# Kernel optimization log

Hardware: AMD Instinct MI355X
Metric: run time of the kernel (lower is better)

Reference implementation:

```python
import jax, jax.numpy as jnp
import numpy as np
from jax import lax

DX, DY, T, B, NMC, HID = 128, 64, 50, 128, 100, 64
PROC_SD, EMIT_SD, LOC_R = 0.05, 0.1, 5.0


def gaspari_cohn(radius, d):
    # static construction (numpy), matches construct_Gaspari_Cohn
    def G(z):
        if 0 <= z < 1:
            return 1.0 - 5.0/3*z**2 + 5.0/8*z**3 + 0.5*z**4 - 0.25*z**5
        elif 1 <= z < 2:
            return 4.0 - 5.0*z + 5.0/3*z**2 + 5.0/8*z**3 - 0.5*z**4 + 1.0/12*z**5 - 2.0/(3.0*z)
        return 0.0
    t = np.zeros((d, d), dtype=np.float32)
    for i in range(d):
        for j in range(d):
            dist = min(abs(i - j), d - abs(i - j))
            t[i, j] = G(dist / radius)
    return jnp.asarray(t)


def setup_inputs():
    key = jax.random.key(0)
    ks = jax.random.split(key, 16)
    rn = lambda k, s, sc=0.05: (jax.random.normal(k, s) * sc).astype(jnp.float32)
    return {
        'observations': jax.random.normal(ks[0], (B, T, DY), jnp.float32),
        'W1': rn(ks[1], (128, DX)), 'b1': jnp.zeros((128,), jnp.float32),
        'W2': rn(ks[2], (64, 128)), 'b2': jnp.zeros((64,), jnp.float32),
        'W3': rn(ks[3], (32, 64)), 'b3': jnp.zeros((32,), jnp.float32),
        'W4': rn(ks[4], (DX, 32)), 'b4': jnp.zeros((DX,), jnp.float32),
        'Wih': rn(ks[5], (4 * HID, DY)), 'Whh': rn(ks[6], (4 * HID, HID)), 'bih': jnp.zeros((4 * HID,), jnp.float32),
        'Wm': rn(ks[7], (DX, HID)), 'bm': jnp.zeros((DX,), jnp.float32),
        'Wv': rn(ks[8], (DX, HID)), 'bv': jnp.zeros((DX,), jnp.float32),
        'eps0': jax.random.normal(ks[9], (NMC, B, DX), jnp.float32),
        'eps_seq': jax.random.normal(ks[10], (T, NMC, B, DX), jnp.float32),
        'noise_y': jax.random.normal(ks[11], (T, B, DY), jnp.float32),
    }


def _forward(observations, W1, b1, W2, b2, W3, b3, W4, b4,
             Wih, Whh, bih, Wm, bm, Wv, bv, eps0, eps_seq, noise_y):
    dt = observations.dtype
    taper = gaspari_cohn(LOC_R, DX).astype(dt)        # [dx, dx]
    Hm = jnp.eye(DX, dtype=dt)[:DY]                    # [dy, dx] emission matrix
    R = (EMIT_SD ** 2) * jnp.eye(DY, dtype=dt)         # observation noise cov

    def mlp(x):  # Four_Layer_NN, relu, no residual
        h = jax.nn.relu(x @ W1.T + b1)
        h = jax.nn.relu(h @ W2.T + b2)
        h = jax.nn.relu(h @ W3.T + b3)
        return h @ W4.T + b4

    # ---- LSTM recognition net -> q(x0) (diagonal MVN) ----
    def lstm_step(carry, x_t):
        h, c = carry
        g = x_t @ Wih.T + h @ Whh.T + bih
        i, f, gg, o = jnp.split(g, 4, axis=-1)
        c = jax.nn.sigmoid(f) * c + jax.nn.sigmoid(i) * jnp.tanh(gg)
        h = jax.nn.sigmoid(o) * jnp.tanh(c)
        return (h, c), None
    h0 = jnp.zeros((B, HID), dt)
    (h_last, _), _ = lax.scan(lstm_step, (h0, h0), jnp.moveaxis(observations, 1, 0))
    q_mean = h_last @ Wm.T + bm                          # [B, dx]
    q_var = jax.nn.softplus(h_last @ Wv.T + bv) + 1e-4   # [B, dx]

    # KL[ q(x0) || N(0, I) ], diagonal covariance
    kl = 0.5 * jnp.sum(q_var + q_mean ** 2 - 1.0 - jnp.log(q_var), axis=-1).mean()

    # rsample ensemble x0: [NMC, B, dx]
    x0 = q_mean[None] + jnp.sqrt(q_var)[None] * eps0

    log2pi = jnp.log(2 * jnp.asarray(np.pi, dt))

    def enkf_step(x_prev, inp):
        y_t, eps_t, ny_t = inp                            # [B,dy], [NMC,B,dx], [B,dy]
        # NN prediction + process noise
        x_t = mlp(x_prev) + eps_t * PROC_SD               # [NMC, B, dx]
        X = jnp.moveaxis(x_t, 0, 1)                       # [B, NMC, dx]
        Xm = X.mean(axis=1, keepdims=True)                # [B, 1, dx]
        Xc = X - Xm
        # localized ensemble covariance (var_inflation = 0)
        P = taper * (jnp.einsum('bnd,bne->bde', Xc, Xc) / (NMC - 1))  # [B, dx, dx]
        # perturbed observations (chol(R) diagonal)
        y_pert = y_t + ny_t * EMIT_SD                     # [B, dy]
        HX = jnp.einsum('bnd,od->bno', X, Hm)             # [B, NMC, dy]
        HP = jnp.einsum('od,bde->boe', Hm, P)             # [B, dy, dx]
        S = jnp.einsum('boe,pe->bop', HP, Hm) + R         # [B, dy, dy]
        L = jnp.linalg.cholesky(S)
        K = jax.scipy.linalg.cho_solve((L, True), HP)     # [B, dy, dx] = S^-1 HP
        X_post = X + jnp.einsum('bno,boe->bne', y_pert[:, None, :] - HX, K)
        HXm = jnp.einsum('bkd,od->bko', Xm, Hm)           # [B, 1, dy]
        Xm_post = Xm + jnp.einsum('bko,boe->bke', y_t[:, None, :] - HXm, K)
        # EnKF marginal log-likelihood N(y | H Xm, S)
        r = y_t - HXm[:, 0, :]
        z = jax.scipy.linalg.solve_triangular(L, r[..., None], lower=True)[..., 0]
        ll = (-0.5 * jnp.sum(z ** 2, -1)
              - jnp.sum(jnp.log(jnp.diagonal(L, axis1=-2, axis2=-1)), -1)
              - 0.5 * DY * log2pi)
        return jnp.moveaxis(X_post, 0, 1), (ll.mean(), Xm_post[:, 0, :])

    xs = (jnp.moveaxis(observations, 1, 0), eps_seq, noise_y)
    _, (lls, means) = lax.scan(enkf_step, x0, xs)
    elbo = -kl + jnp.sum(lls)
    return elbo, means  # means: [T, B, dx] posterior ensemble means


def reference(observations, W1, b1, W2, b2, W3, b3, W4, b4,
              Wih, Whh, bih, Wm, bm, Wv, bv, eps0, eps_seq, noise_y):
    return _forward(observations, W1, b1, W2, b2, W3, b3, W4, b4,
                    Wih, Whh, bih, Wm, bm, Wv, bv, eps0, eps_seq, noise_y)
```

## Files before the change

kernel.cpp:

```cpp
#include <hip/hip_runtime.h>

#define TC   50
#define BC   128
#define DXC  128
#define DYC  64
#define NMCC 100
#define XBS  136
#define A1S  136
#define A2S  72
#define A3S  40
#define IVS  72
#define KTS  72
#define HPS  20
#define LBS  12
#define ZSS  67

typedef float f32x4 __attribute__((ext_vector_type(4)));
typedef short s16x8 __attribute__((ext_vector_type(8)));

__device__ __forceinline__ unsigned short f2bf(float x){
  unsigned int u = __float_as_uint(x);
  u += 0x7fffu + ((u >> 16) & 1u);
  return (unsigned short)(u >> 16);
}

__device__ __forceinline__ unsigned int pk2bf(float lo, float hi){
  unsigned int r;
  asm volatile("v_cvt_pk_bf16_f32 %0, %1, %2" : "=v"(r) : "v"(lo), "v"(hi));
  return r;
}

__device__ __forceinline__ f32x4 mfma16(s16x8 a, s16x8 b, f32x4 c){
  return __builtin_amdgcn_mfma_f32_16x16x32_bf16(a, b, c, 0, 0, 0);
}

__device__ __forceinline__ s16x8 packA8(const float* p){
  f32x4 a = *(const f32x4*)p;
  f32x4 c = *(const f32x4*)(p + 4);
  s16x8 r;
  r[0]=(short)f2bf(a[0]); r[1]=(short)f2bf(a[1]);
  r[2]=(short)f2bf(a[2]); r[3]=(short)f2bf(a[3]);
  r[4]=(short)f2bf(c[0]); r[5]=(short)f2bf(c[1]);
  r[6]=(short)f2bf(c[2]); r[7]=(short)f2bf(c[3]);
  return r;
}

__device__ __forceinline__ float gc_taper(int row, int col){
  int dd = row - col; if (dd < 0) dd = -dd;
  if (128 - dd < dd) dd = 128 - dd;
  double z = (double)dd / 5.0;
  double g = 0.0;
  if (z < 1.0){
    g = 1.0 - (5.0/3.0)*z*z + (5.0/8.0)*z*z*z + 0.5*z*z*z*z - 0.25*z*z*z*z*z;
  } else if (z < 2.0){
    g = 4.0 - 5.0*z + (5.0/3.0)*z*z + (5.0/8.0)*z*z*z - 0.5*z*z*z*z
        + (1.0/12.0)*z*z*z*z*z - 2.0/(3.0*z);
  }
  return (float)(g / 99.0);
}

__global__ __launch_bounds__(256) void gin_kernel(const float* __restrict__ obs,
                          const float* __restrict__ Wih, const float* __restrict__ bih,
                          float* __restrict__ gin){
  __shared__ float xrow[64];
  int blk = blockIdx.x;
  int t = blk / BC, b = blk % BC;
  int tid = threadIdx.x;
  if (tid < 64) xrow[tid] = obs[(b*TC + t)*DYC + tid];
  __syncthreads();
  float s = bih[tid];
  #pragma unroll
  for (int k = 0; k < 64; k += 4){
    f32x4 wv = *(const f32x4*)&Wih[tid*64 + k];
    s += wv[0]*xrow[k] + wv[1]*xrow[k+1] + wv[2]*xrow[k+2] + wv[3]*xrow[k+3];
  }
  gin[blk*256 + tid] = s;
}

__global__ __launch_bounds__(256,1) void lstm_kernel(const float* __restrict__ gin,
     const float* __restrict__ Whh,
     const float* __restrict__ Wm, const float* __restrict__ bm,
     const float* __restrict__ Wv, const float* __restrict__ bv,
     float* __restrict__ qmean, float* __restrict__ qstd, float* __restrict__ klp){
  __shared__ float h[64], cc[64], graw[256], red[128];
  int b = blockIdx.x, tid = threadIdx.x;
  float w[64];
  #pragma unroll
  for (int k = 0; k < 64; k += 4){
    f32x4 v = *(const f32x4*)&Whh[tid*64 + k];
    w[k]=v[0]; w[k+1]=v[1]; w[k+2]=v[2]; w[k+3]=v[3];
  }
  if (tid < 64){ h[tid] = 0.f; cc[tid] = 0.f; }
  __syncthreads();
  for (int t = 0; t < TC; ++t){
    float g = gin[(t*BC + b)*256 + tid];
    #pragma unroll
    for (int k = 0; k < 64; k += 4){
      f32x4 hv = *(const f32x4*)&h[k];
      g += hv[0]*w[k] + hv[1]*w[k+1] + hv[2]*w[k+2] + hv[3]*w[k+3];
    }
    graw[tid] = g;
    __syncthreads();
    if (tid < 64){
      float ig = 1.f/(1.f + expf(-graw[tid]));
      float fg = 1.f/(1.f + expf(-graw[64 + tid]));
      float gg = tanhf(graw[128 + tid]);
      float og = 1.f/(1.f + expf(-graw[192 + tid]));
      float cn = fg*cc[tid] + ig*gg;
      cc[tid] = cn;
      h[tid] = og*tanhf(cn);
    }
    __syncthreads();
  }
  if (tid < 128){
    float sm_ = bm[tid], sv_ = bv[tid];
    #pragma unroll
    for (int k = 0; k < 64; k += 4){
      f32x4 wmv = *(const f32x4*)&Wm[tid*64 + k];
      f32x4 wvv = *(const f32x4*)&Wv[tid*64 + k];
      f32x4 hv  = *(const f32x4*)&h[k];
      sm_ += wmv[0]*hv[0] + wmv[1]*hv[1] + wmv[2]*hv[2] + wmv[3]*hv[3];
      sv_ += wvv[0]*hv[0] + wvv[1]*hv[1] + wvv[2]*hv[2] + wvv[3]*hv[3];
    }
    float qv = ((sv_ > 20.f) ? sv_ : log1pf(expf(sv_))) + 1e-4f;
    qmean[b*DXC + tid] = sm_;
    qstd[b*DXC + tid]  = sqrtf(qv);
    red[tid] = 0.5f*(qv + sm_*sm_ - 1.f - logf(qv));
  }
  __syncthreads();
  if (tid == 0){
    float s = 0.f;
    for (int i = 0; i < 128; ++i) s += red[i];
    klp[b] = s;
  }
}

__global__ __launch_bounds__(512,1) void enkf_kernel(
    const float* __restrict__ obs,
    const float* __restrict__ W1, const float* __restrict__ b1g,
    const float* __restrict__ W2, const float* __restrict__ b2g,
    const float* __restrict__ W3, const float* __restrict__ b3g,
    const float* __restrict__ W4, const float* __restrict__ b4g,
    const float* __restrict__ eps0, const float* __restrict__ epss,
    const float* __restrict__ nsyg,
    const float* __restrict__ qmean, const float* __restrict__ qstd,
    float* __restrict__ out_means, float* __restrict__ llp)
{
  __shared__ unsigned short sU[128*XBS];
  __shared__ unsigned short sA[112*A1S];
  __shared__ unsigned short sB[112*A2S];
  __shared__ unsigned short sC[112*A3S];
  __shared__ float sHPb[64*HPS];
  __shared__ float sW9[9*12];
  __shared__ float sLb[64*LBS];
  __shared__ float sXm[DXC];
  __shared__ float sRv[DYC];
  __shared__ float sSc[4];

  const int b    = blockIdx.x;
  const int tid  = threadIdx.x;
  const int lane = tid & 63;
  const int wid  = tid >> 6;
  const int l15  = lane & 15;
  const int l4   = lane >> 4;

  const int colN = wid*16 + l15;
  const int col2 = (wid & 3)*16 + l15;
  const int col3 = (wid & 1)*16 + l15;
  const int m02  = (wid >> 2) * 4;
  const int mc2  = (wid >> 2) ? 3 : 4;
  const int m03  = (wid >> 1) * 2;
  const int mc3  = ((wid >> 1) == 3) ? 1 : 2;

  s16x8 w1f[4], w2f[4], w3f[2], w4f;
  #pragma unroll
  for (int kt = 0; kt < 4; ++kt) w1f[kt] = packA8(&W1[colN*128 + kt*32 + 8*l4]);
  #pragma unroll
  for (int kt = 0; kt < 4; ++kt) w2f[kt] = packA8(&W2[col2*128 + kt*32 + 8*l4]);
  #pragma unroll
  for (int kt = 0; kt < 2; ++kt) w3f[kt] = packA8(&W3[col3*64 + kt*32 + 8*l4]);
  w4f = packA8(&W4[colN*32 + 8*l4]);
  const float bb1 = b1g[colN], bb2 = b2g[col2], bb3 = b3g[col3], bb4 = b4g[colN];

  const int mt1 = (0x22111000u >> (4*wid)) & 15;
  const int nt1 = (0x21210710u >> (4*wid)) & 15;
  const int mt2 = (0x3332u >> (4*wid)) & 15;
  const int nt2 = (0x4323u >> (4*wid)) & 15;
  float tv1[4], tv2[4];
  #pragma unroll
  for (int i = 0; i < 4; ++i){
    tv1[i] = gc_taper(mt1*16 + 4*l4 + i, nt1*16 + l15);
    tv2[i] = (wid < 4) ? gc_taper(mt2*16 + 4*l4 + i, nt2*16 + l15) : 0.f;
  }

  int cdk = 10, cdd = 0;
  { int acc = 0;
    #pragma unroll
    for (int q = 0; q < 10; ++q){
      int cnt = 10 - q;
      if (lane >= acc && lane < acc + cnt){ cdk = q; cdd = lane - acc; }
      acc += cnt;
    } }
  const int ioff_s  = (cdk + cdd > 9) ? 0 : (cdk + cdd);
  const int dk_s    = (cdk > 9) ? 0 : cdk;
  int baseNext = (cdk + 1)*10 - ((cdk + 1)*cdk)/2;
  const int shsrc   = (baseNext + cdd >= 55) ? 0 : (baseNext + cdd);
  const bool enterSlot = (cdk + cdd == 9) && (cdk <= 9);
  const bool isCol0    = (cdk == 0);

  float xreg[7][4];
  {
    float qm = qmean[b*DXC + colN], qs = qstd[b*DXC + colN];
    #pragma unroll
    for (int m = 0; m < 7; ++m)
      #pragma unroll
      for (int i = 0; i < 4; ++i){
        int row = m*16 + 4*l4 + i;
        float v = 0.f;
        if (row < NMCC) v = qm + qs * eps0[((size_t)row*BC + b)*DXC + colN];
        xreg[m][i] = v;
        if (row < NMCC) sU[row*XBS + colN] = f2bf(v);
      }
    for (int idx = tid; idx < 12*128; idx += 512)
      sU[(100 + (idx >> 7))*XBS + (idx & 127)] = 0;
  }
  float ev[7][4];
  #pragma unroll
  for (int m = 0; m < 7; ++m)
    #pragma unroll
    for (int i = 0; i < 4; ++i){
      int row = m*16 + 4*l4 + i;
      ev[m][i] = (row < NMCC) ? epss[((size_t)row*BC + b)*DXC + colN] : 0.f;
    }
  __syncthreads();

  float llsum = 0.f;
  const f32x4 z4 = {0.f, 0.f, 0.f, 0.f};

  for (int t = 0; t < TC; ++t){
    float ldet_t = 0.f;

    float y_r = 0.f, ypv = 0.f;
    if (wid < 4){
      y_r = obs[((size_t)b*TC + t)*DYC + colN];
      ypv = y_r + 0.1f*nsyg[((size_t)t*BC + b)*DYC + colN];
    }

    {
      f32x4 acc[7];
      #pragma unroll
      for (int m = 0; m < 7; ++m) acc[m] = z4;
      #pragma unroll
      for (int kt = 0; kt < 4; ++kt){
        #pragma unroll
        for (int m = 0; m < 7; ++m){
          s16x8 af = *(const s16x8*)&sU[(m*16 + l15)*XBS + kt*32 + 8*l4];
          acc[m] = mfma16(af, w1f[kt], acc[m]);
        }
      }
      #pragma unroll
      for (int m = 0; m < 7; ++m)
        #pragma unroll
        for (int i = 0; i < 4; ++i){
          int row = m*16 + 4*l4 + i;
          sA[row*A1S + colN] = f2bf(fmaxf(acc[m][i] + bb1, 0.f));
        }
    }
    __syncthreads();

    {
      f32x4 acc[4];
      #pragma unroll
      for (int mm = 0; mm < 4; ++mm) acc[mm] = z4;
      #pragma unroll
      for (int kt = 0; kt < 4; ++kt){
        #pragma unroll
        for (int mm = 0; mm < 4; ++mm){
          if (mm < mc2){
            s16x8 af = *(const s16x8*)&sA[((m02+mm)*16 + l15)*A1S + kt*32 + 8*l4];
            acc[mm] = mfma16(af, w2f[kt], acc[mm]);
          }
        }
      }
      #pragma unroll
      for (int mm = 0; mm < 4; ++mm){
        if (mm < mc2){
          #pragma unroll
          for (int i = 0; i < 4; ++i){
            int row = (m02+mm)*16 + 4*l4 + i;
            sB[row*A2S + col2] = f2bf(fmaxf(acc[mm][i] + bb2, 0.f));
          }
        }
      }
    }
    __syncthreads();

    {
      f32x4 acc[2];
      acc[0] = z4; acc[1] = z4;
      #pragma unroll
      for (int kt = 0; kt < 2; ++kt){
        #pragma unroll
        for (int mm = 0; mm < 2; ++mm){
          if (mm < mc3){
            s16x8 af = *(const s16x8*)&sB[((m03+mm)*16 + l15)*A2S + kt*32 + 8*l4];
            acc[mm] = mfma16(af, w3f[kt], acc[mm]);
          }
        }
      }
      #pragma unroll
      for (int mm = 0; mm < 2; ++mm){
        if (mm < mc3){
          #pragma unroll
          for (int i = 0; i < 4; ++i){
            int row = (m03+mm)*16 + 4*l4 + i;
            sC[row*A3S + col3] = f2bf(fmaxf(acc[mm][i] + bb3, 0.f));
          }
        }
      }
    }
    __syncthreads();

    {
      f32x4 acc[7];
      #pragma unroll
      for (int m = 0; m < 7; ++m) acc[m] = z4;
      #pragma unroll
      for (int m = 0; m < 7; ++m){
        s16x8 af = *(const s16x8*)&sC[(m*16 + l15)*A3S + 8*l4];
        acc[m] = mfma16(af, w4f, acc[m]);
      }
      float part = 0.f;
      #pragma unroll
      for (int m = 0; m < 7; ++m)
        #pragma unroll
        for (int i = 0; i < 4; ++i){
          int row = m*16 + 4*l4 + i;
          if (row < NMCC){
            float v = acc[m][i] + bb4 + 0.05f*ev[m][i];
            xreg[m][i] = v;
            part += v;
          } else xreg[m][i] = 0.f;
        }
      part += __shfl_xor(part, 16);
      part += __shfl_xor(part, 32);
      float xm = part * 0.01f;
      if (l4 == 0) sXm[colN] = xm;
      if (wid < 4 && l4 == 0) sRv[colN] = y_r - xm;

      if (colN <= 72 || colN >= 119){
        #pragma unroll
        for (int m = 0; m < 7; ++m){
          float v0, v1, v2, v3;
          if (m == 6 && l4 > 0){ v0 = v1 = v2 = v3 = 0.f; }
          else {
            v0 = xreg[m][0] - xm; v1 = xreg[m][1] - xm;
            v2 = xreg[m][2] - xm; v3 = xreg[m][3] - xm;
          }
          uint2 pk;
          pk.x = pk2bf(v0, v1);
          pk.y = pk2bf(v2, v3);
          *(uint2*)&sU[colN*XBS + m*16 + 4*l4] = pk;
        }
        uint2 zz; zz.x = 0u; zz.y = 0u;
        *(uint2*)&sU[colN*XBS + 112 + 4*l4] = zz;
      }
      if (wid == 0){
        #pragma unroll
        for (int m = 0; m < 7; ++m)
          #pragma unroll
          for (int i = 0; i < 4; ++i){
            int row = m*16 + 4*l4 + i;
            sB[row*IVS + colN] = (row < NMCC) ? f2bf(ypv - xreg[m][i])
                                              : (unsigned short)0;
          }
      }
    }
    __syncthreads();

    {
      f32x4 a1 = z4, a2 = z4;
      #pragma unroll
      for (int kt = 0; kt < 4; ++kt){
        s16x8 fa1 = *(const s16x8*)&sU[(mt1*16 + l15)*XBS + kt*32 + 8*l4];
        s16x8 fb1 = *(const s16x8*)&sU[(nt1*16 + l15)*XBS + kt*32 + 8*l4];
        a1 = mfma16(fa1, fb1, a1);
        if (wid < 4){
          s16x8 fa2 = *(const s16x8*)&sU[(mt2*16 + l15)*XBS + kt*32 + 8*l4];
          s16x8 fb2 = *(const s16x8*)&sU[(nt2*16 + l15)*XBS + kt*32 + 8*l4];
          a2 = mfma16(fa2, fb2, a2);
        }
      }
      #pragma unroll
      for (int i = 0; i < 4; ++i){
        int o = mt1*16 + 4*l4 + i, e = nt1*16 + l15;
        float v = a1[i] * tv1[i];
        if (nt1 != 7){
          int dd = e - o;
          if (dd >= -9 && dd <= 9) sHPb[o*HPS + dd + 9] = v;
        } else {
          int w = e - 119;
          if (w >= 0 && o <= w) sW9[o*12 + w] = v;
        }
      }
      if (wid < 4){
        #pragma unroll
        for (int i = 0; i < 4; ++i){
          int o = mt2*16 + 4*l4 + i, e = nt2*16 + l15;
          float v = a2[i] * tv2[i];
          int dd = e - o;
          if (dd >= -9 && dd <= 9) sHPb[o*HPS + dd + 9] = v;
        }
      }
    }
    __syncthreads();

    if (t + 1 < TC){
      #pragma unroll
      for (int m = 0; m < 7; ++m)
        #pragma unroll
        for (int i = 0; i < 4; ++i){
          int row = m*16 + 4*l4 + i;
          if (row < NMCC)
            ev[m][i] = epss[((size_t)((t+1)*NMCC + row)*BC + b)*DXC + colN];
        }
    }
    if (wid == 0){
      float v = 0.f;
      if (cdk <= 9) v = sHPb[cdk*HPS + cdd + 9] + ((cdd == 0) ? 0.01f : 0.f);
      for (int j = 0; j < 64; ++j){
        float enter = 0.f;
        if (enterSlot && (j + 10 < 64))
          enter = sHPb[(j + 10 - cdd)*HPS + cdd + 9] + ((cdd == 0) ? 0.01f : 0.f);
        float upiv = __shfl(v, 0);
        float u1   = __shfl(v, ioff_s);
        float u2   = __shfl(v, dk_s);
        float rd   = rsqrtf(upiv);
        float rpiv = rd * rd;
        if (isCol0){
          sLb[j*LBS + cdd] = (cdd == 0) ? rd : v * rd;
        }
        if (lane == 0) ldet_t += 0.5f * logf(upiv);
        float vu = (cdk >= 1) ? v - u1*u2*rpiv : v;
        float vs = __shfl(vu, shsrc);
        v = enterSlot ? enter : vs;
      }
    } else if (wid < 4){
      #pragma unroll
      for (int m = 0; m < 7; ++m)
        #pragma unroll
        for (int i = 0; i < 4; ++i){
          int row = m*16 + 4*l4 + i;
          sB[row*IVS + colN] = (row < NMCC) ? f2bf(ypv - xreg[m][i])
                                            : (unsigned short)0;
        }
    }
    __syncthreads();

    {
      float* zscr = (float*)sU;
      unsigned short* KT = (unsigned short*)sA;
      int c = tid;
      if (c < 83){
        int e = (c < 73) ? c : (c + 46);
        bool isr = (c == 82);
        float w0,w1,w2,w3,w4,w5,w6,w7,w8,w9;
        {
          float wi[10];
          #pragma unroll
          for (int d = 0; d < 10; ++d){
            float bv = 0.f;
            if (isr) bv = sRv[d];
            else if (c < 73){
              int idx = e - d + 9;
              if (idx >= 0 && idx <= 18) bv = sHPb[d*HPS + idx];
            } else {
              int ww = e - 119;
              if (d <= ww) bv = sW9[d*12 + ww];
            }
            wi[d] = bv;
          }
          w0=wi[0]; w1=wi[1]; w2=wi[2]; w3=wi[3]; w4=wi[4];
          w5=wi[5]; w6=wi[6]; w7=wi[7]; w8=wi[8]; w9=wi[9];
        }
        float z2l = 0.f;
        for (int j = 0; j < 64; ++j){
          f32x4 lb0 = *(const f32x4*)&sLb[j*LBS];
          f32x4 lb4 = *(const f32x4*)&sLb[j*LBS + 4];
          float  l8 = sLb[j*LBS + 8], l9 = sLb[j*LBS + 9];
          float z = w0 * lb0[0];
          zscr[c*ZSS + j] = z;
          z2l += z*z;
          w0 = w1 - lb0[1]*z; w1 = w2 - lb0[2]*z; w2 = w3 - lb0[3]*z;
          w3 = w4 - lb4[0]*z; w4 = w5 - lb4[1]*z; w5 = w6 - lb4[2]*z;
          w6 = w7 - lb4[3]*z; w7 = w8 - l8*z;     w8 = w9 - l9*z;
          int jn = j + 10;
          float bv = 0.f;
          if (isr){ if (jn < 64) bv = sRv[jn]; }
          else if (c < 73){
            if (jn < 64 && j >= e - 19 && j <= e - 1) bv = sHPb[jn*HPS + (e - j - 1)];
          }
          w9 = bv;
        }
        if (isr) sSc[0] = z2l;
        float x1=0.f,x2=0.f,x3=0.f,x4=0.f,x5=0.f,x6=0.f,x7=0.f,x8=0.f,x9=0.f;
        float macc = 0.f, xodd = 0.f;
        for (int j = 63; j >= 0; --j){
          f32x4 lb0 = *(const f32x4*)&sLb[j*LBS];
          f32x4 lb4 = *(const f32x4*)&sLb[j*LBS + 4];
          float  l8 = sLb[j*LBS + 8], l9 = sLb[j*LBS + 9];
          float acc = zscr[c*ZSS + j]
            - lb0[1]*x1 - lb0[2]*x2 - lb0[3]*x3
            - lb4[0]*x4 - lb4[1]*x5 - lb4[2]*x6 - lb4[3]*x7
            - l8*x8 - l9*x9;
          float xj = acc * lb0[0];
          if (!isr){
            macc += sRv[j]*xj;
            if (j & 1) xodd = xj;
            else *(unsigned int*)&KT[e*KTS + j] = pk2bf(xj, xodd);
          }
          x9=x8; x8=x7; x7=x6; x6=x5; x5=x4; x4=x3; x3=x2; x2=x1; x1=xj;
        }
        if (!isr) out_means[((size_t)t*BC + b)*DXC + e] = sXm[e] + macc;
      } else if (c < 129){
        int e = c - 10;
        out_means[((size_t)t*BC + b)*DXC + e] = sXm[e];
      }
    }
    __syncthreads();

    if (tid == 0){
      llsum += -0.5f*sSc[0] - ldet_t - 58.812066f;
    }
    {
      f32x4 uacc[7];
      #pragma unroll
      for (int m = 0; m < 7; ++m) uacc[m] = z4;
      if (wid != 5 && wid != 6){
        const unsigned short* KT = (const unsigned short*)sA;
        #pragma unroll
        for (int kt = 0; kt < 2; ++kt){
          s16x8 bf = *(const s16x8*)&KT[colN*KTS + kt*32 + 8*l4];
          #pragma unroll
          for (int m = 0; m < 7; ++m){
            s16x8 af = *(const s16x8*)&sB[(m*16 + l15)*IVS + kt*32 + 8*l4];
            uacc[m] = mfma16(af, bf, uacc[m]);
          }
        }
      }
      bool upd = ((colN <= 72) || (colN >= 119)) && (wid != 5) && (wid != 6);
      #pragma unroll
      for (int m = 0; m < 7; ++m)
        #pragma unroll
        for (int i = 0; i < 4; ++i){
          int row = m*16 + 4*l4 + i;
          if (row < NMCC){
            float xn = xreg[m][i] + (upd ? uacc[m][i] : 0.f);
            xreg[m][i] = xn;
            sU[row*XBS + colN] = f2bf(xn);
          }
        }
    }
    __syncthreads();
  }

  if (tid == 0) llp[b] = llsum;
}

__global__ void final_kernel(const float* __restrict__ klp, const float* __restrict__ llp,
                             float* __restrict__ out){
  __shared__ float s1[128], s2[128];
  int tid = threadIdx.x;
  s1[tid] = klp[tid];
  s2[tid] = llp[tid];
  __syncthreads();
  if (tid == 0){
    float a = 0.f, c = 0.f;
    for (int i = 0; i < 128; ++i){ a += s1[i]; c += s2[i]; }
    out[0] = -a/128.f + c/128.f;
  }
}

extern "C" void kernel_launch(void* const* d_in, const int* in_sizes, int n_in,
                              void* d_out, int out_size, void* d_ws, size_t ws_size,
                              hipStream_t stream){
  (void)in_sizes; (void)n_in; (void)out_size; (void)ws_size;
  const float* obs  = (const float*)d_in[0];
  const float* W1   = (const float*)d_in[1];
  const float* b1   = (const float*)d_in[2];
  const float* W2   = (const float*)d_in[3];
  const float* b2   = (const float*)d_in[4];
  const float* W3   = (const float*)d_in[5];
  const float* b3   = (const float*)d_in[6];
  const float* W4   = (const float*)d_in[7];
  const float* b4   = (const float*)d_in[8];
  const float* Wih  = (const float*)d_in[9];
  const float* Whh  = (const float*)d_in[10];
  const float* bih  = (const float*)d_in[11];
  const float* Wm   = (const float*)d_in[12];
  const float* bm   = (const float*)d_in[13];
  const float* Wv   = (const float*)d_in[14];
  const float* bv   = (const float*)d_in[15];
  const float* eps0 = (const float*)d_in[16];
  const float* epss = (const float*)d_in[17];
  const float* nsy  = (const float*)d_in[18];

  char* ws = (char*)d_ws;
  float* gin   = (float*)(ws + 0);
  float* qmean = (float*)(ws + 6553600);
  float* qstd  = (float*)(ws + 6619136);
  float* klp   = (float*)(ws + 6684672);
  float* llp   = (float*)(ws + 6685184);

  float* out = (float*)d_out;

  hipLaunchKernelGGL(gin_kernel, dim3(TC*BC), dim3(256), 0, stream,
                     obs, Wih, bih, gin);
  hipLaunchKernelGGL(lstm_kernel, dim3(BC), dim3(256), 0, stream,
                     gin, Whh, Wm, bm, Wv, bv, qmean, qstd, klp);
  hipLaunchKernelGGL(enkf_kernel, dim3(BC), dim3(512), 0, stream,
                     obs, W1, b1, W2, b2, W3, b3, W4, b4,
                     eps0, epss, nsy, qmean, qstd, out + 1, llp);
  hipLaunchKernelGGL(final_kernel, dim3(1), dim3(128), 0, stream, klp, llp, out);
}
```

Measured before the change: 1.985 ms.

## Double EnKF block to 1024 threads and spread MLP and covariance tiles across waves

Launches the EnKF kernel with 16 waves instead of 8. The first MLP layer's M tiles are split across two wave groups, layers 2 and 3 use finer per-wave tiles, and the covariance MFMA tiles get one tile per wave, so each wave's serial chain of MFMAs in those phases is shorter. W2 and W3 are now staged once in LDS as bf16 rather than held in registers, and the l8/l9 pair is read as a single float2. The cost is more LDS use, extra LDS reads of weight fragments, and a register budget halved per thread at 1024 threads (launch_bounds 1024), which risks spills given the large xreg/ev arrays. Eight waves also sit idle in several phases while still paying for every barrier.

```diff
diff --git a/kernel.cpp b/kernel.cpp
--- a/kernel.cpp
+++ b/kernel.cpp
@@ -14,6 +14,8 @@
 #define HPS  20
 #define LBS  12
 #define ZSS  67
+#define W2S  136
+#define W3S  72
 
 typedef float f32x4 __attribute__((ext_vector_type(4)));
 typedef short s16x8 __attribute__((ext_vector_type(8)));
@@ -135,7 +137,7 @@
   }
 }
 
-__global__ __launch_bounds__(512,1) void enkf_kernel(
+__global__ __launch_bounds__(1024,1) void enkf_kernel(
     const float* __restrict__ obs,
     const float* __restrict__ W1, const float* __restrict__ b1g,
     const float* __restrict__ W2, const float* __restrict__ b2g,
@@ -150,6 +152,8 @@
   __shared__ unsigned short sA[112*A1S];
   __shared__ unsigned short sB[112*A2S];
   __shared__ unsigned short sC[112*A3S];
+  __shared__ unsigned short sW2[64*W2S];
+  __shared__ unsigned short sW3[32*W3S];
   __shared__ float sHPb[64*HPS];
   __shared__ float sW9[9*12];
   __shared__ float sLb[64*LBS];
@@ -164,34 +168,27 @@
   const int l15  = lane & 15;
   const int l4   = lane >> 4;
 
-  const int colN = wid*16 + l15;
+  const int colN = (wid & 7)*16 + l15;
   const int col2 = (wid & 3)*16 + l15;
   const int col3 = (wid & 1)*16 + l15;
-  const int m02  = (wid >> 2) * 4;
-  const int mc2  = (wid >> 2) ? 3 : 4;
-  const int m03  = (wid >> 1) * 2;
-  const int mc3  = ((wid >> 1) == 3) ? 1 : 2;
-
-  s16x8 w1f[4], w2f[4], w3f[2], w4f;
+  const int mb1  = (wid >> 3) * 4;
+  const int mc1  = (wid >> 3) ? 3 : 4;
+  const int mb2  = (wid >> 2 & 3) * 2;
+  const int mc2  = ((wid >> 2 & 3) == 3) ? 1 : 2;
+  const int mt3  = (wid >> 1) & 7;
+
+  s16x8 w1f[4], w4f;
   #pragma unroll
   for (int kt = 0; kt < 4; ++kt) w1f[kt] = packA8(&W1[colN*128 + kt*32 + 8*l4]);
-  #pragma unroll
-  for (int kt = 0; kt < 4; ++kt) w2f[kt] = packA8(&W2[col2*128 + kt*32 + 8*l4]);
-  #pragma unroll
-  for (int kt = 0; kt < 2; ++kt) w3f[kt] = packA8(&W3[col3*64 + kt*32 + 8*l4]);
   w4f = packA8(&W4[colN*32 + 8*l4]);
   const float bb1 = b1g[colN], bb2 = b2g[col2], bb3 = b3g[col3], bb4 = b4g[colN];
 
-  const int mt1 = (0x22111000u >> (4*wid)) & 15;
-  const int nt1 = (0x21210710u >> (4*wid)) & 15;
-  const int mt2 = (0x3332u >> (4*wid)) & 15;
-  const int nt2 = (0x4323u >> (4*wid)) & 15;
-  float tv1[4], tv2[4];
+  const int mtw = (int)((0x333222111000ull >> (4*wid)) & 15);
+  const int ntw = (int)((0x432321210710ull >> (4*wid)) & 15);
+  float tv[4];
   #pragma unroll
-  for (int i = 0; i < 4; ++i){
-    tv1[i] = gc_taper(mt1*16 + 4*l4 + i, nt1*16 + l15);
-    tv2[i] = (wid < 4) ? gc_taper(mt2*16 + 4*l4 + i, nt2*16 + l15) : 0.f;
-  }
+  for (int i = 0; i < 4; ++i)
+    tv[i] = gc_taper(mtw*16 + 4*l4 + i, ntw*16 + l15);
 
   int cdk = 10, cdd = 0;
   { int acc = 0;
@@ -208,8 +205,13 @@
   const bool enterSlot = (cdk + cdd == 9) && (cdk <= 9);
   const bool isCol0    = (cdk == 0);
 
+  for (int idx = tid; idx < 64*128; idx += 1024)
+    sW2[(idx >> 7)*W2S + (idx & 127)] = f2bf(W2[idx]);
+  for (int idx = tid; idx < 32*64; idx += 1024)
+    sW3[(idx >> 6)*W3S + (idx & 63)] = f2bf(W3[idx]);
+
   float xreg[7][4];
-  {
+  if (wid < 8){
     float qm = qmean[b*DXC + colN], qs = qstd[b*DXC + colN];
     #pragma unroll
     for (int m = 0; m < 7; ++m)
@@ -221,17 +223,25 @@
         xreg[m][i] = v;
         if (row < NMCC) sU[row*XBS + colN] = f2bf(v);
       }
-    for (int idx = tid; idx < 12*128; idx += 512)
-      sU[(100 + (idx >> 7))*XBS + (idx & 127)] = 0;
-  }
+  } else {
+    #pragma unroll
+    for (int m = 0; m < 7; ++m)
+      #pragma unroll
+      for (int i = 0; i < 4; ++i) xreg[m][i] = 0.f;
+  }
+  for (int idx = tid; idx < 12*128; idx += 1024)
+    sU[(100 + (idx >> 7))*XBS + (idx & 127)] = 0;
+
   float ev[7][4];
-  #pragma unroll
-  for (int m = 0; m < 7; ++m)
+  if (wid < 8){
     #pragma unroll
-    for (int i = 0; i < 4; ++i){
-      int row = m*16 + 4*l4 + i;
-      ev[m][i] = (row < NMCC) ? epss[((size_t)row*BC + b)*DXC + colN] : 0.f;
-    }
+    for (int m = 0; m < 7; ++m)
+      #pragma unroll
+      for (int i = 0; i < 4; ++i){
+        int row = m*16 + 4*l4 + i;
+        ev[m][i] = (row < NMCC) ? epss[((size_t)row*BC + b)*DXC + colN] : 0.f;
+      }
+  }
   __syncthreads();
 
   float llsum = 0.f;
@@ -247,47 +257,52 @@
     }
 
     {
-      f32x4 acc[7];
-      #pragma unroll
-      for (int m = 0; m < 7; ++m) acc[m] = z4;
+      f32x4 acc[4];
+      #pragma unroll
+      for (int mm = 0; mm < 4; ++mm) acc[mm] = z4;
       #pragma unroll
       for (int kt = 0; kt < 4; ++kt){
         #pragma unroll
-        for (int m = 0; m < 7; ++m){
-          s16x8 af = *(const s16x8*)&sU[(m*16 + l15)*XBS + kt*32 + 8*l4];
-          acc[m] = mfma16(af, w1f[kt], acc[m]);
-        }
-      }
-      #pragma unroll
-      for (int m = 0; m < 7; ++m)
-        #pragma unroll
-        for (int i = 0; i < 4; ++i){
-          int row = m*16 + 4*l4 + i;
-          sA[row*A1S + colN] = f2bf(fmaxf(acc[m][i] + bb1, 0.f));
-        }
+        for (int mm = 0; mm < 4; ++mm){
+          if (mm < mc1){
+            s16x8 af = *(const s16x8*)&sU[((mb1+mm)*16 + l15)*XBS + kt*32 + 8*l4];
+            acc[mm] = mfma16(af, w1f[kt], acc[mm]);
+          }
+        }
+      }
+      #pragma unroll
+      for (int mm = 0; mm < 4; ++mm){
+        if (mm < mc1){
+          #pragma unroll
+          for (int i = 0; i < 4; ++i){
+            int row = (mb1+mm)*16 + 4*l4 + i;
+            sA[row*A1S + colN] = f2bf(fmaxf(acc[mm][i] + bb1, 0.f));
+          }
+        }
+      }
     }
     __syncthreads();
 
     {
-      f32x4 acc[4];
-      #pragma unroll
-      for (int mm = 0; mm < 4; ++mm) acc[mm] = z4;
+      f32x4 acc[2];
+      acc[0] = z4; acc[1] = z4;
       #pragma unroll
       for (int kt = 0; kt < 4; ++kt){
-        #pragma unroll
-        for (int mm = 0; mm < 4; ++mm){
+        s16x8 bf = *(const s16x8*)&sW2[col2*W2S + kt*32 + 8*l4];
+        #pragma unroll
+        for (int mm = 0; mm < 2; ++mm){
           if (mm < mc2){
-            s16x8 af = *(const s16x8*)&sA[((m02+mm)*16 + l15)*A1S + kt*32 + 8*l4];
-            acc[mm] = mfma16(af, w2f[kt], acc[mm]);
-          }
-        }
-      }
-      #pragma unroll
-      for (int mm = 0; mm < 4; ++mm){
+            s16x8 af = *(const s16x8*)&sA[((mb2+mm)*16 + l15)*A1S + kt*32 + 8*l4];
+            acc[mm] = mfma16(af, bf, acc[mm]);
+          }
+        }
+      }
+      #pragma unroll
+      for (int mm = 0; mm < 2; ++mm){
         if (mm < mc2){
           #pragma unroll
           for (int i = 0; i < 4; ++i){
-            int row = (m02+mm)*16 + 4*l4 + i;
+            int row = (mb2+mm)*16 + 4*l4 + i;
             sB[row*A2S + col2] = f2bf(fmaxf(acc[mm][i] + bb2, 0.f));
           }
         }
@@ -295,33 +310,23 @@
     }
     __syncthreads();
 
-    {
-      f32x4 acc[2];
-      acc[0] = z4; acc[1] = z4;
+    if (mt3 < 7){
+      f32x4 acc = z4;
       #pragma unroll
       for (int kt = 0; kt < 2; ++kt){
-        #pragma unroll
-        for (int mm = 0; mm < 2; ++mm){
-          if (mm < mc3){
-            s16x8 af = *(const s16x8*)&sB[((m03+mm)*16 + l15)*A2S + kt*32 + 8*l4];
-            acc[mm] = mfma16(af, w3f[kt], acc[mm]);
-          }
-        }
-      }
-      #pragma unroll
-      for (int mm = 0; mm < 2; ++mm){
-        if (mm < mc3){
-          #pragma unroll
-          for (int i = 0; i < 4; ++i){
-            int row = (m03+mm)*16 + 4*l4 + i;
-            sC[row*A3S + col3] = f2bf(fmaxf(acc[mm][i] + bb3, 0.f));
-          }
-        }
-      }
-    }
-    __syncthreads();
-
-    {
+        s16x8 bf = *(const s16x8*)&sW3[col3*W3S + kt*32 + 8*l4];
+        s16x8 af = *(const s16x8*)&sB[(mt3*16 + l15)*A2S + kt*32 + 8*l4];
+        acc = mfma16(af, bf, acc);
+      }
+      #pragma unroll
+      for (int i = 0; i < 4; ++i){
+        int row = mt3*16 + 4*l4 + i;
+        sC[row*A3S + col3] = f2bf(fmaxf(acc[i] + bb3, 0.f));
+      }
+    }
+    __syncthreads();
+
+    if (wid < 8){
       f32x4 acc[7];
       #pragma unroll
       for (int m = 0; m < 7; ++m) acc[m] = z4;
@@ -378,24 +383,19 @@
     }
     __syncthreads();
 
-    {
-      f32x4 a1 = z4, a2 = z4;
+    if (wid < 12){
+      f32x4 a1 = z4;
       #pragma unroll
       for (int kt = 0; kt < 4; ++kt){
-        s16x8 fa1 = *(const s16x8*)&sU[(mt1*16 + l15)*XBS + kt*32 + 8*l4];
-        s16x8 fb1 = *(const s16x8*)&sU[(nt1*16 + l15)*XBS + kt*32 + 8*l4];
-        a1 = mfma16(fa1, fb1, a1);
-        if (wid < 4){
-          s16x8 fa2 = *(const s16x8*)&sU[(mt2*16 + l15)*XBS + kt*32 + 8*l4];
-          s16x8 fb2 = *(const s16x8*)&sU[(nt2*16 + l15)*XBS + kt*32 + 8*l4];
-          a2 = mfma16(fa2, fb2, a2);
-        }
+        s16x8 fa = *(const s16x8*)&sU[(mtw*16 + l15)*XBS + kt*32 + 8*l4];
+        s16x8 fb = *(const s16x8*)&sU[(ntw*16 + l15)*XBS + kt*32 + 8*l4];
+        a1 = mfma16(fa, fb, a1);
       }
       #pragma unroll
       for (int i = 0; i < 4; ++i){
-        int o = mt1*16 + 4*l4 + i, e = nt1*16 + l15;
-        float v = a1[i] * tv1[i];
-        if (nt1 != 7){
+        int o = mtw*16 + 4*l4 + i, e = ntw*16 + l15;
+        float v = a1[i] * tv[i];
+        if (ntw != 7){
           int dd = e - o;
           if (dd >= -9 && dd <= 9) sHPb[o*HPS + dd + 9] = v;
         } else {
@@ -403,19 +403,10 @@
           if (w >= 0 && o <= w) sW9[o*12 + w] = v;
         }
       }
-      if (wid < 4){
-        #pragma unroll
-        for (int i = 0; i < 4; ++i){
-          int o = mt2*16 + 4*l4 + i, e = nt2*16 + l15;
-          float v = a2[i] * tv2[i];
-          int dd = e - o;
-          if (dd >= -9 && dd <= 9) sHPb[o*HPS + dd + 9] = v;
-        }
-      }
-    }
-    __syncthreads();
-
-    if (t + 1 < TC){
+    }
+    __syncthreads();
+
+    if (wid < 8 && t + 1 < TC){
       #pragma unroll
       for (int m = 0; m < 7; ++m)
         #pragma unroll
@@ -487,13 +478,13 @@
         for (int j = 0; j < 64; ++j){
           f32x4 lb0 = *(const f32x4*)&sLb[j*LBS];
           f32x4 lb4 = *(const f32x4*)&sLb[j*LBS + 4];
-          float  l8 = sLb[j*LBS + 8], l9 = sLb[j*LBS + 9];
+          float2 l89 = *(const float2*)&sLb[j*LBS + 8];
           float z = w0 * lb0[0];
           zscr[c*ZSS + j] = z;
           z2l += z*z;
           w0 = w1 - lb0[1]*z; w1 = w2 - lb0[2]*z; w2 = w3 - lb0[3]*z;
           w3 = w4 - lb4[0]*z; w4 = w5 - lb4[1]*z; w5 = w6 - lb4[2]*z;
-          w6 = w7 - lb4[3]*z; w7 = w8 - l8*z;     w8 = w9 - l9*z;
+          w6 = w7 - lb4[3]*z; w7 = w8 - l89.x*z;  w8 = w9 - l89.y*z;
           int jn = j + 10;
           float bv = 0.f;
           if (isr){ if (jn < 64) bv = sRv[jn]; }
@@ -508,11 +499,11 @@
         for (int j = 63; j >= 0; --j){
           f32x4 lb0 = *(const f32x4*)&sLb[j*LBS];
           f32x4 lb4 = *(const f32x4*)&sLb[j*LBS + 4];
-          float  l8 = sLb[j*LBS + 8], l9 = sLb[j*LBS + 9];
+          float2 l89 = *(const float2*)&sLb[j*LBS + 8];
           float acc = zscr[c*ZSS + j]
             - lb0[1]*x1 - lb0[2]*x2 - lb0[3]*x3
             - lb4[0]*x4 - lb4[1]*x5 - lb4[2]*x6 - lb4[3]*x7
-            - l8*x8 - l9*x9;
+            - l89.x*x8 - l89.y*x9;
           float xj = acc * lb0[0];
           if (!isr){
             macc += sRv[j]*xj;
@@ -532,7 +523,7 @@
     if (tid == 0){
       llsum += -0.5f*sSc[0] - ldet_t - 58.812066f;
     }
-    {
+    if (wid < 8){
       f32x4 uacc[7];
       #pragma unroll
       for (int m = 0; m < 7; ++m) uacc[m] = z4;
@@ -618,7 +609,7 @@
                      obs, Wih, bih, gin);
   hipLaunchKernelGGL(lstm_kernel, dim3(BC), dim3(256), 0, stream,
                      gin, Whh, Wm, bm, Wv, bv, qmean, qstd, klp);
-  hipLaunchKernelGGL(enkf_kernel, dim3(BC), dim3(512), 0, stream,
+  hipLaunchKernelGGL(enkf_kernel, dim3(BC), dim3(1024), 0, stream,
                      obs, W1, b1, W2, b2, W3, b3, W4, b4,
                      eps0, epss, nsy, qmean, qstd, out + 1, llp);
   hipLaunchKernelGGL(final_kernel, dim3(1), dim3(128), 0, stream, klp, llp, out);
```

New measurement: 2.529 ms. 1.27x slower.

## Fuse MLP layers 2-3 per row-wave with LDS weights, prefetch solve operands

Applied to the files above, without the earlier changes.

Layers 2 and 3 of the MLP now run back-to-back in each of seven row-tile waves, with W2/W3 staged once in LDS as bf16, which removes one block barrier per time step. The eps loads move to the start of each step instead of being prefetched at the end, the Cholesky wave gets raised scheduling priority, and the forward/back triangular solves software-prefetch the next L row and z value. This adds LDS footprint and redundant weight reads from LDS, and the eps loads now sit closer to their use, exposing their latency.

```diff
diff --git a/kernel.cpp b/kernel.cpp
--- a/kernel.cpp
+++ b/kernel.cpp
@@ -14,6 +14,8 @@
 #define HPS  20
 #define LBS  12
 #define ZSS  67
+#define W2S  136
+#define W3S  72
 
 typedef float f32x4 __attribute__((ext_vector_type(4)));
 typedef short s16x8 __attribute__((ext_vector_type(8)));
@@ -150,6 +152,8 @@
   __shared__ unsigned short sA[112*A1S];
   __shared__ unsigned short sB[112*A2S];
   __shared__ unsigned short sC[112*A3S];
+  __shared__ unsigned short sW2[64*W2S];
+  __shared__ unsigned short sW3[32*W3S];
   __shared__ float sHPb[64*HPS];
   __shared__ float sW9[9*12];
   __shared__ float sLb[64*LBS];
@@ -165,22 +169,18 @@
   const int l4   = lane >> 4;
 
   const int colN = wid*16 + l15;
-  const int col2 = (wid & 3)*16 + l15;
-  const int col3 = (wid & 1)*16 + l15;
-  const int m02  = (wid >> 2) * 4;
-  const int mc2  = (wid >> 2) ? 3 : 4;
-  const int m03  = (wid >> 1) * 2;
-  const int mc3  = ((wid >> 1) == 3) ? 1 : 2;
-
-  s16x8 w1f[4], w2f[4], w3f[2], w4f;
+  const int rw   = wid;
+
+  s16x8 w1f[4], w4f;
   #pragma unroll
   for (int kt = 0; kt < 4; ++kt) w1f[kt] = packA8(&W1[colN*128 + kt*32 + 8*l4]);
+  w4f = packA8(&W4[colN*32 + 8*l4]);
+  const float bb1 = b1g[colN], bb4 = b4g[colN];
+  float bb2v[4], bb3v[2];
   #pragma unroll
-  for (int kt = 0; kt < 4; ++kt) w2f[kt] = packA8(&W2[col2*128 + kt*32 + 8*l4]);
+  for (int cg = 0; cg < 4; ++cg) bb2v[cg] = b2g[cg*16 + l15];
   #pragma unroll
-  for (int kt = 0; kt < 2; ++kt) w3f[kt] = packA8(&W3[col3*64 + kt*32 + 8*l4]);
-  w4f = packA8(&W4[colN*32 + 8*l4]);
-  const float bb1 = b1g[colN], bb2 = b2g[col2], bb3 = b3g[col3], bb4 = b4g[colN];
+  for (int cg = 0; cg < 2; ++cg) bb3v[cg] = b3g[cg*16 + l15];
 
   const int mt1 = (0x22111000u >> (4*wid)) & 15;
   const int nt1 = (0x21210710u >> (4*wid)) & 15;
@@ -208,6 +208,11 @@
   const bool enterSlot = (cdk + cdd == 9) && (cdk <= 9);
   const bool isCol0    = (cdk == 0);
 
+  for (int idx = tid; idx < 64*128; idx += 512)
+    sW2[(idx >> 7)*W2S + (idx & 127)] = f2bf(W2[idx]);
+  for (int idx = tid; idx < 32*64; idx += 512)
+    sW3[(idx >> 6)*W3S + (idx & 63)] = f2bf(W3[idx]);
+
   float xreg[7][4];
   {
     float qm = qmean[b*DXC + colN], qs = qstd[b*DXC + colN];
@@ -224,14 +229,6 @@
     for (int idx = tid; idx < 12*128; idx += 512)
       sU[(100 + (idx >> 7))*XBS + (idx & 127)] = 0;
   }
-  float ev[7][4];
-  #pragma unroll
-  for (int m = 0; m < 7; ++m)
-    #pragma unroll
-    for (int i = 0; i < 4; ++i){
-      int row = m*16 + 4*l4 + i;
-      ev[m][i] = (row < NMCC) ? epss[((size_t)row*BC + b)*DXC + colN] : 0.f;
-    }
   __syncthreads();
 
   float llsum = 0.f;
@@ -246,6 +243,16 @@
       ypv = y_r + 0.1f*nsyg[((size_t)t*BC + b)*DYC + colN];
     }
 
+    float ev[7][4];
+    #pragma unroll
+    for (int m = 0; m < 7; ++m)
+      #pragma unroll
+      for (int i = 0; i < 4; ++i){
+        int row = m*16 + 4*l4 + i;
+        ev[m][i] = (row < NMCC)
+          ? epss[((size_t)(t*NMCC + row)*BC + b)*DXC + colN] : 0.f;
+      }
+
     {
       f32x4 acc[7];
       #pragma unroll
@@ -268,56 +275,44 @@
     }
     __syncthreads();
 
-    {
-      f32x4 acc[4];
-      #pragma unroll
-      for (int mm = 0; mm < 4; ++mm) acc[mm] = z4;
+    if (rw < 7){
+      f32x4 a2[4];
+      #pragma unroll
+      for (int cg = 0; cg < 4; ++cg) a2[cg] = z4;
       #pragma unroll
       for (int kt = 0; kt < 4; ++kt){
-        #pragma unroll
-        for (int mm = 0; mm < 4; ++mm){
-          if (mm < mc2){
-            s16x8 af = *(const s16x8*)&sA[((m02+mm)*16 + l15)*A1S + kt*32 + 8*l4];
-            acc[mm] = mfma16(af, w2f[kt], acc[mm]);
-          }
-        }
-      }
-      #pragma unroll
-      for (int mm = 0; mm < 4; ++mm){
-        if (mm < mc2){
-          #pragma unroll
-          for (int i = 0; i < 4; ++i){
-            int row = (m02+mm)*16 + 4*l4 + i;
-            sB[row*A2S + col2] = f2bf(fmaxf(acc[mm][i] + bb2, 0.f));
-          }
-        }
-      }
-    }
-    __syncthreads();
-
-    {
-      f32x4 acc[2];
-      acc[0] = z4; acc[1] = z4;
+        s16x8 af = *(const s16x8*)&sA[(16*rw + l15)*A1S + kt*32 + 8*l4];
+        #pragma unroll
+        for (int cg = 0; cg < 4; ++cg){
+          s16x8 bf = *(const s16x8*)&sW2[(cg*16 + l15)*W2S + kt*32 + 8*l4];
+          a2[cg] = mfma16(af, bf, a2[cg]);
+        }
+      }
+      #pragma unroll
+      for (int cg = 0; cg < 4; ++cg)
+        #pragma unroll
+        for (int i = 0; i < 4; ++i){
+          int row = 16*rw + 4*l4 + i;
+          sB[row*A2S + cg*16 + l15] = f2bf(fmaxf(a2[cg][i] + bb2v[cg], 0.f));
+        }
+      f32x4 a3[2];
+      a3[0] = z4; a3[1] = z4;
       #pragma unroll
       for (int kt = 0; kt < 2; ++kt){
-        #pragma unroll
-        for (int mm = 0; mm < 2; ++mm){
-          if (mm < mc3){
-            s16x8 af = *(const s16x8*)&sB[((m03+mm)*16 + l15)*A2S + kt*32 + 8*l4];
-            acc[mm] = mfma16(af, w3f[kt], acc[mm]);
-          }
-        }
-      }
-      #pragma unroll
-      for (int mm = 0; mm < 2; ++mm){
-        if (mm < mc3){
-          #pragma unroll
-          for (int i = 0; i < 4; ++i){
-            int row = (m03+mm)*16 + 4*l4 + i;
-            sC[row*A3S + col3] = f2bf(fmaxf(acc[mm][i] + bb3, 0.f));
-          }
-        }
-      }
+        s16x8 af3 = *(const s16x8*)&sB[(16*rw + l15)*A2S + kt*32 + 8*l4];
+        #pragma unroll
+        for (int cg = 0; cg < 2; ++cg){
+          s16x8 bf = *(const s16x8*)&sW3[(cg*16 + l15)*W3S + kt*32 + 8*l4];
+          a3[cg] = mfma16(af3, bf, a3[cg]);
+        }
+      }
+      #pragma unroll
+      for (int cg = 0; cg < 2; ++cg)
+        #pragma unroll
+        for (int i = 0; i < 4; ++i){
+          int row = 16*rw + 4*l4 + i;
+          sC[row*A3S + cg*16 + l15] = f2bf(fmaxf(a3[cg][i] + bb3v[cg], 0.f));
+        }
     }
     __syncthreads();
 
@@ -415,17 +410,8 @@
     }
     __syncthreads();
 
-    if (t + 1 < TC){
-      #pragma unroll
-      for (int m = 0; m < 7; ++m)
-        #pragma unroll
-        for (int i = 0; i < 4; ++i){
-          int row = m*16 + 4*l4 + i;
-          if (row < NMCC)
-            ev[m][i] = epss[((size_t)((t+1)*NMCC + row)*BC + b)*DXC + colN];
-        }
-    }
     if (wid == 0){
+      __builtin_amdgcn_s_setprio(1);
       float v = 0.f;
       if (cdk <= 9) v = sHPb[cdk*HPS + cdd + 9] + ((cdd == 0) ? 0.01f : 0.f);
       for (int j = 0; j < 64; ++j){
@@ -445,6 +431,7 @@
         float vs = __shfl(vu, shsrc);
         v = enterSlot ? enter : vs;
       }
+      __builtin_amdgcn_s_setprio(0);
     } else if (wid < 4){
       #pragma unroll
       for (int m = 0; m < 7; ++m)
@@ -484,16 +471,22 @@
           w5=wi[5]; w6=wi[6]; w7=wi[7]; w8=wi[8]; w9=wi[9];
         }
         float z2l = 0.f;
+        f32x4 lb0 = *(const f32x4*)&sLb[0];
+        f32x4 lb4 = *(const f32x4*)&sLb[4];
+        float2 l89 = *(const float2*)&sLb[8];
         for (int j = 0; j < 64; ++j){
-          f32x4 lb0 = *(const f32x4*)&sLb[j*LBS];
-          f32x4 lb4 = *(const f32x4*)&sLb[j*LBS + 4];
-          float  l8 = sLb[j*LBS + 8], l9 = sLb[j*LBS + 9];
+          f32x4 nb0 = lb0, nb4 = lb4; float2 n89 = l89;
+          if (j + 1 < 64){
+            nb0 = *(const f32x4*)&sLb[(j+1)*LBS];
+            nb4 = *(const f32x4*)&sLb[(j+1)*LBS + 4];
+            n89 = *(const float2*)&sLb[(j+1)*LBS + 8];
+          }
           float z = w0 * lb0[0];
           zscr[c*ZSS + j] = z;
           z2l += z*z;
           w0 = w1 - lb0[1]*z; w1 = w2 - lb0[2]*z; w2 = w3 - lb0[3]*z;
           w3 = w4 - lb4[0]*z; w4 = w5 - lb4[1]*z; w5 = w6 - lb4[2]*z;
-          w6 = w7 - lb4[3]*z; w7 = w8 - l8*z;     w8 = w9 - l9*z;
+          w6 = w7 - lb4[3]*z; w7 = w8 - l89.x*z;  w8 = w9 - l89.y*z;
           int jn = j + 10;
           float bv = 0.f;
           if (isr){ if (jn < 64) bv = sRv[jn]; }
@@ -501,18 +494,28 @@
             if (jn < 64 && j >= e - 19 && j <= e - 1) bv = sHPb[jn*HPS + (e - j - 1)];
           }
           w9 = bv;
+          lb0 = nb0; lb4 = nb4; l89 = n89;
         }
         if (isr) sSc[0] = z2l;
         float x1=0.f,x2=0.f,x3=0.f,x4=0.f,x5=0.f,x6=0.f,x7=0.f,x8=0.f,x9=0.f;
         float macc = 0.f, xodd = 0.f;
+        lb0 = *(const f32x4*)&sLb[63*LBS];
+        lb4 = *(const f32x4*)&sLb[63*LBS + 4];
+        l89 = *(const float2*)&sLb[63*LBS + 8];
+        float zcur = zscr[c*ZSS + 63];
         for (int j = 63; j >= 0; --j){
-          f32x4 lb0 = *(const f32x4*)&sLb[j*LBS];
-          f32x4 lb4 = *(const f32x4*)&sLb[j*LBS + 4];
-          float  l8 = sLb[j*LBS + 8], l9 = sLb[j*LBS + 9];
-          float acc = zscr[c*ZSS + j]
+          f32x4 nb0 = lb0, nb4 = lb4; float2 n89 = l89;
+          float znext = zcur;
+          if (j > 0){
+            nb0 = *(const f32x4*)&sLb[(j-1)*LBS];
+            nb4 = *(const f32x4*)&sLb[(j-1)*LBS + 4];
+            n89 = *(const float2*)&sLb[(j-1)*LBS + 8];
+            znext = zscr[c*ZSS + j - 1];
+          }
+          float acc = zcur
             - lb0[1]*x1 - lb0[2]*x2 - lb0[3]*x3
             - lb4[0]*x4 - lb4[1]*x5 - lb4[2]*x6 - lb4[3]*x7
-            - l8*x8 - l9*x9;
+            - l89.x*x8 - l89.y*x9;
           float xj = acc * lb0[0];
           if (!isr){
             macc += sRv[j]*xj;
@@ -520,6 +523,7 @@
             else *(unsigned int*)&KT[e*KTS + j] = pk2bf(xj, xodd);
           }
           x9=x8; x8=x7; x7=x6; x6=x5; x5=x4; x4=x3; x3=x2; x2=x1; x1=xj;
+          lb0 = nb0; lb4 = nb4; l89 = n89; zcur = znext;
         }
         if (!isr) out_means[((size_t)t*BC + b)*DXC + e] = sXm[e] + macc;
       } else if (c < 129){
```

Result: slower. 2.041 ms (median of 2 runs) (+2.8%).
